# Optimization experiments

Hardware: AMD Instinct MI355X
Metric: run time of the kernel (lower is better)

The kernel has to match this reference:

```python
import jax, jax.numpy as jnp
import numpy as np

N_NODES = 20000
N_EDGES = 320000
N_QUERY = 100000
D = 256


def _sage_conv(x, adj_row, adj_col, Wl, bl, Wr):
    # PyG SAGEConv with mean aggregation over SparseTensor adj_t:
    #   out = lin_l(mean_{j in N(i)} x_j) + lin_r(x_i)
    # adj_row = destination node, adj_col = source node.
    n = x.shape[0]
    msg = x[adj_col]                                        # [E, D] gather
    agg = jax.ops.segment_sum(msg, adj_row, num_segments=n)  # [N, D]
    deg = jax.ops.segment_sum(jnp.ones((adj_row.shape[0],), x.dtype), adj_row,
                              num_segments=n)
    agg = agg / jnp.maximum(deg, 1.0)[:, None]               # mean reduce
    return agg @ Wl + bl + x @ Wr


def setup_inputs() -> dict:
    key = jax.random.key(0)
    ks = jax.random.split(key, 12)
    s = 1.0 / np.sqrt(D)
    return {
        "adj_row": jax.random.randint(ks[0], (N_EDGES,), 0, N_NODES, dtype=jnp.int32),
        "adj_col": jax.random.randint(ks[1], (N_EDGES,), 0, N_NODES, dtype=jnp.int32),
        "edges": jax.random.randint(ks[2], (2, N_QUERY), 0, N_NODES, dtype=jnp.int32),
        "emb": jax.random.normal(ks[3], (N_NODES, D), jnp.float32),
        "W1l": jax.random.normal(ks[4], (D, D), jnp.float32) * s,
        "b1": jnp.zeros((D,), jnp.float32),
        "W1r": jax.random.normal(ks[5], (D, D), jnp.float32) * s,
        "W2l": jax.random.normal(ks[6], (D, D), jnp.float32) * s,
        "b2": jnp.zeros((D,), jnp.float32),
        "W2r": jax.random.normal(ks[7], (D, D), jnp.float32) * s,
        "Wp1": jax.random.normal(ks[8], (D, D), jnp.float32) * s,
        "bp1": jnp.zeros((D,), jnp.float32),
        "Wp2": jax.random.normal(ks[9], (D, 1), jnp.float32) * s,
        "bp2": jnp.zeros((1,), jnp.float32),
    }


def reference(adj_row, adj_col, edges, emb, W1l, b1, W1r, W2l, b2, W2r,
              Wp1, bp1, Wp2, bp2):
    # SAGE backbone (eval mode: dropout is identity)
    x = _sage_conv(emb, adj_row, adj_col, W1l, b1, W1r)
    x = jax.nn.relu(x)
    x = _sage_conv(x, adj_row, adj_col, W2l, b2, W2r)     # [N, D]
    # LinkPredictor: h = x_i * x_j -> MLP -> sigmoid
    h = x[edges[0]] * x[edges[1]]                          # [Q, D]
    h = jax.nn.relu(h @ Wp1 + bp1)
    return jax.nn.sigmoid(h @ Wp2 + bp2)                   # [Q, 1]
```

## Files before the change

kernel.cpp:

```cpp
#include <hip/hip_runtime.h>
#include <cstddef>

constexpr int NN = 20000;
constexpr int NE = 320000;
constexpr int NQ = 100000;
constexpr int DD = 256;
constexpr int NB = (NN + 255) / 256;
constexpr int CASTB = (NN * DD / 8 + 255) / 256;

typedef __attribute__((ext_vector_type(8))) short bf16x8;
typedef __attribute__((ext_vector_type(4))) float f32x4;
typedef __attribute__((ext_vector_type(4))) unsigned short u16x4;
typedef __attribute__((ext_vector_type(8))) unsigned short u16x8;

__device__ inline unsigned short f2bf(float f) {
    union { float f; unsigned u; } v; v.f = f;
    unsigned r = v.u + 0x7fffu + ((v.u >> 16) & 1u);
    return (unsigned short)(r >> 16);
}
__device__ inline float bf2f(unsigned short h) {
    union { unsigned u; float f; } t; t.u = ((unsigned)h) << 16;
    return t.f;
}

__global__ __launch_bounds__(256) void k_castpack(
    const float* __restrict__ x, unsigned short* __restrict__ y,
    int* __restrict__ deg, int* __restrict__ bflag,
    const float* __restrict__ w0, const float* __restrict__ w1,
    const float* __restrict__ w2, const float* __restrict__ w3,
    const float* __restrict__ w4,
    unsigned short* __restrict__ h0, unsigned short* __restrict__ h1,
    unsigned short* __restrict__ h2, unsigned short* __restrict__ h3,
    unsigned short* __restrict__ h4,
    unsigned short* __restrict__ l0, unsigned short* __restrict__ l1,
    unsigned short* __restrict__ l2, unsigned short* __restrict__ l3) {
    const int bid = blockIdx.x;
    if (bid < CASTB) {
        int i = bid * 256 + threadIdx.x;
        if (i < NN) deg[i] = 0;
        if (bid == 0 && threadIdx.x < NB) bflag[threadIdx.x] = 0;
        if (i >= NN * DD / 8) return;
        float4 f0 = *reinterpret_cast<const float4*>(x + (size_t)i * 8);
        float4 f1 = *reinterpret_cast<const float4*>(x + (size_t)i * 8 + 4);
        u16x8 o;
        o[0] = f2bf(f0.x); o[1] = f2bf(f0.y); o[2] = f2bf(f0.z); o[3] = f2bf(f0.w);
        o[4] = f2bf(f1.x); o[5] = f2bf(f1.y); o[6] = f2bf(f1.z); o[7] = f2bf(f1.w);
        *reinterpret_cast<u16x8*>(y + (size_t)i * 8) = o;
        return;
    }
    int mb = bid - CASTB;
    int m = mb >> 5;
    int idx = (mb & 31) * 256 + threadIdx.x;
    const float* W = (m == 0) ? w0 : (m == 1) ? w1 : (m == 2) ? w2 : (m == 3) ? w3 : w4;
    unsigned short* H = (m == 0) ? h0 : (m == 1) ? h1 : (m == 2) ? h2 : (m == 3) ? h3 : h4;
    unsigned short* L = (m == 0) ? l0 : (m == 1) ? l1 : (m == 2) ? l2 : (m == 3) ? l3 : nullptr;
    int t = idx >> 6, lane = idx & 63;
    int kt = t >> 4, nt = t & 15;
    int k0 = kt * 32 + (lane >> 4) * 8;
    int n = nt * 16 + (lane & 15);
    unsigned uh[4], ul[4];
#pragma unroll
    for (int i = 0; i < 4; ++i) {
        float fa = W[(size_t)(k0 + 2 * i) * DD + n];
        float fb = W[(size_t)(k0 + 2 * i + 1) * DD + n];
        unsigned short ha = f2bf(fa), hb = f2bf(fb);
        unsigned short la = f2bf(fa - bf2f(ha)), lb = f2bf(fb - bf2f(hb));
        uh[i] = (unsigned)ha | ((unsigned)hb << 16);
        ul[i] = (unsigned)la | ((unsigned)lb << 16);
    }
    *reinterpret_cast<uint4*>(H + (size_t)idx * 8) = make_uint4(uh[0], uh[1], uh[2], uh[3]);
    if (L)
        *reinterpret_cast<uint4*>(L + (size_t)idx * 8) = make_uint4(ul[0], ul[1], ul[2], ul[3]);
}

__global__ __launch_bounds__(256) void k_deg(const int* __restrict__ row,
                                             int* __restrict__ deg) {
    int e = blockIdx.x * 256 + threadIdx.x;
    if (e < NE) atomicAdd(&deg[row[e]], 1);
}

__global__ __launch_bounds__(256) void k_scanf(const int* __restrict__ deg,
                                               int* __restrict__ offs,
                                               int* __restrict__ cursor,
                                               float* __restrict__ recip,
                                               int* __restrict__ bflag) {
    __shared__ int wsum[4];
    __shared__ int s_pre;
    const int tid = threadIdx.x, lane = tid & 63, wid = tid >> 6;
    const int bid = blockIdx.x;
    int i = bid * 256 + tid;
    int v = (i < NN) ? deg[i] : 0;
    int sc = v;
#pragma unroll
    for (int d = 1; d < 64; d <<= 1) {
        int t = __shfl_up(sc, d);
        if (lane >= d) sc += t;
    }
    if (lane == 63) wsum[wid] = sc;
    __syncthreads();
    int wpre = 0;
    for (int w = 0; w < wid; ++w) wpre += wsum[w];
    int btot = wsum[0] + wsum[1] + wsum[2] + wsum[3];

    if (tid == 0) atomicExch(&bflag[bid], btot + 1);

    int myv = 0;
    if (tid < bid) {
        int f;
        do { f = atomicAdd(&bflag[tid], 0); } while (f == 0);
        myv = f - 1;
    }
    int rs = myv;
#pragma unroll
    for (int d = 1; d < 64; d <<= 1) rs += __shfl_xor(rs, d);
    __syncthreads();
    if (lane == 0) wsum[wid] = rs;
    __syncthreads();
    if (tid == 0) s_pre = wsum[0] + wsum[1] + wsum[2] + wsum[3];
    __syncthreads();
    int pre = s_pre;

    if (i < NN) {
        int o = pre + wpre + sc - v;
        offs[i] = o;
        cursor[i] = o;
        recip[i] = 1.0f / fmaxf((float)v, 1.0f);
    }
    if (i == 0) offs[NN] = NE;
}

__global__ __launch_bounds__(256) void k_fill(const int* __restrict__ row,
                                              const int* __restrict__ col,
                                              int* __restrict__ cursor,
                                              int* __restrict__ scol) {
    int e = blockIdx.x * 256 + threadIdx.x;
    if (e < NE) {
        int r = row[e];
        int p = atomicAdd(&cursor[r], 1);
        scol[p] = col[e];
    }
}

__global__ __launch_bounds__(256) void k_lin(
    const unsigned short* __restrict__ A,
    const unsigned short* __restrict__ Wlh, const unsigned short* __restrict__ Wll,
    const unsigned short* __restrict__ Wrh, const unsigned short* __restrict__ Wrl,
    unsigned short* __restrict__ P, unsigned short* __restrict__ Q) {
    const int ns   = blockIdx.x & 7;
    const int mblk = blockIdx.x >> 3;
    const int wave = threadIdx.x >> 6;
    const int lane = threadIdx.x & 63;
    const int row0 = mblk * 128 + wave * 32;
    const int kcol = (lane >> 4) * 8;
    const int ar0 = min(row0 + (lane & 15), NN - 1);
    const int ar1 = min(row0 + 16 + (lane & 15), NN - 1);

    f32x4 accP[2][2], accQ[2][2];
#pragma unroll
    for (int mt = 0; mt < 2; ++mt)
#pragma unroll
        for (int nt = 0; nt < 2; ++nt) {
            accP[mt][nt] = {0, 0, 0, 0};
            accQ[mt][nt] = {0, 0, 0, 0};
        }

#pragma unroll 2
    for (int kt = 0; kt < 8; ++kt) {
        bf16x8 a0 = *reinterpret_cast<const bf16x8*>(A + (size_t)ar0 * DD + kt * 32 + kcol);
        bf16x8 a1 = *reinterpret_cast<const bf16x8*>(A + (size_t)ar1 * DD + kt * 32 + kcol);
#pragma unroll
        for (int nt = 0; nt < 2; ++nt) {
            const size_t fo = ((size_t)((kt * 16 + ns * 2 + nt) * 64 + lane)) * 8;
            bf16x8 blh = *reinterpret_cast<const bf16x8*>(Wlh + fo);
            bf16x8 bll = *reinterpret_cast<const bf16x8*>(Wll + fo);
            bf16x8 brh = *reinterpret_cast<const bf16x8*>(Wrh + fo);
            bf16x8 brl = *reinterpret_cast<const bf16x8*>(Wrl + fo);
            __builtin_amdgcn_s_setprio(1);
            accP[0][nt] = __builtin_amdgcn_mfma_f32_16x16x32_bf16(a0, blh, accP[0][nt], 0, 0, 0);
            accP[1][nt] = __builtin_amdgcn_mfma_f32_16x16x32_bf16(a1, blh, accP[1][nt], 0, 0, 0);
            accP[0][nt] = __builtin_amdgcn_mfma_f32_16x16x32_bf16(a0, bll, accP[0][nt], 0, 0, 0);
            accP[1][nt] = __builtin_amdgcn_mfma_f32_16x16x32_bf16(a1, bll, accP[1][nt], 0, 0, 0);
            accQ[0][nt] = __builtin_amdgcn_mfma_f32_16x16x32_bf16(a0, brh, accQ[0][nt], 0, 0, 0);
            accQ[1][nt] = __builtin_amdgcn_mfma_f32_16x16x32_bf16(a1, brh, accQ[1][nt], 0, 0, 0);
            accQ[0][nt] = __builtin_amdgcn_mfma_f32_16x16x32_bf16(a0, brl, accQ[0][nt], 0, 0, 0);
            accQ[1][nt] = __builtin_amdgcn_mfma_f32_16x16x32_bf16(a1, brl, accQ[1][nt], 0, 0, 0);
            __builtin_amdgcn_s_setprio(0);
        }
    }

    const int n0 = lane & 15;
    const int rg = (lane >> 4) * 4;
#pragma unroll
    for (int mt = 0; mt < 2; ++mt)
#pragma unroll
        for (int nt = 0; nt < 2; ++nt) {
            int n = (ns * 2 + nt) * 16 + n0;
#pragma unroll
            for (int j = 0; j < 4; ++j) {
                int r = row0 + mt * 16 + rg + j;
                if (r < NN) {
                    P[(size_t)r * DD + n] = f2bf(accP[mt][nt][j]);
                    Q[(size_t)r * DD + n] = f2bf(accQ[mt][nt][j]);
                }
            }
        }
}

template <int RELU>
__global__ __launch_bounds__(256) void k_gath(const int* __restrict__ offs,
                                              const int* __restrict__ scol,
                                              const float* __restrict__ recip,
                                              const unsigned short* __restrict__ P,
                                              const unsigned short* __restrict__ Q,
                                              const float* __restrict__ b,
                                              unsigned short* __restrict__ out) {
    int node = blockIdx.x * 4 + (threadIdx.x >> 6);
    int lane = threadIdx.x & 63;
    if (node >= NN) return;
    int s = offs[node];
    int e = offs[node + 1];
    const int half = lane >> 5;
    const int l32 = lane & 31;
    float a0[8] = {0,0,0,0,0,0,0,0}, a1[8] = {0,0,0,0,0,0,0,0};
    float a2[8] = {0,0,0,0,0,0,0,0}, a3[8] = {0,0,0,0,0,0,0,0};
    int p = s;
    for (; p + 7 < e; p += 8) {
        int base = p + 4 * half;
        int c0 = scol[base], c1 = scol[base + 1], c2 = scol[base + 2], c3 = scol[base + 3];
        u16x8 v0 = *reinterpret_cast<const u16x8*>(P + (size_t)c0 * DD + l32 * 8);
        u16x8 v1 = *reinterpret_cast<const u16x8*>(P + (size_t)c1 * DD + l32 * 8);
        u16x8 v2 = *reinterpret_cast<const u16x8*>(P + (size_t)c2 * DD + l32 * 8);
        u16x8 v3 = *reinterpret_cast<const u16x8*>(P + (size_t)c3 * DD + l32 * 8);
#pragma unroll
        for (int i = 0; i < 8; ++i) {
            a0[i] += bf2f(v0[i]); a1[i] += bf2f(v1[i]);
            a2[i] += bf2f(v2[i]); a3[i] += bf2f(v3[i]);
        }
    }
    for (; p + 1 < e; p += 2) {
        int c0 = scol[p + half];
        u16x8 v0 = *reinterpret_cast<const u16x8*>(P + (size_t)c0 * DD + l32 * 8);
#pragma unroll
        for (int i = 0; i < 8; ++i) a0[i] += bf2f(v0[i]);
    }
    if (p < e && half == 0) {
        int c0 = scol[p];
        u16x8 v0 = *reinterpret_cast<const u16x8*>(P + (size_t)c0 * DD + l32 * 8);
#pragma unroll
        for (int i = 0; i < 8; ++i) a1[i] += bf2f(v0[i]);
    }
    float rc = recip[node];
    u16x8 q = *reinterpret_cast<const u16x8*>(Q + (size_t)node * DD + l32 * 8);
    float4 b0 = *reinterpret_cast<const float4*>(b + l32 * 8);
    float4 b1 = *reinterpret_cast<const float4*>(b + l32 * 8 + 4);
    float bb[8] = {b0.x, b0.y, b0.z, b0.w, b1.x, b1.y, b1.z, b1.w};
    u16x8 o;
#pragma unroll
    for (int i = 0; i < 8; ++i) {
        float t = a0[i] + a1[i] + a2[i] + a3[i];
        t += __shfl_xor(t, 32);
        t = t * rc + bf2f(q[i]) + bb[i];
        if (RELU) t = fmaxf(t, 0.0f);
        o[i] = f2bf(t);
    }
    if (half == 0)
        *reinterpret_cast<u16x8*>(out + (size_t)node * DD + l32 * 8) = o;
}

__global__ __launch_bounds__(512, 4) void k_pred(const int* __restrict__ edges,
                                                 const unsigned short* __restrict__ x2,
                                                 const unsigned short* __restrict__ Wp1p,
                                                 const float* __restrict__ bp1,
                                                 const float* __restrict__ Wp2,
                                                 const float* __restrict__ bp2,
                                                 float* __restrict__ out) {
    __shared__ unsigned short sh[128 * 256];
    const int tid = threadIdx.x;
    const int wave = tid >> 6;
    const int lane = tid & 63;
    const int q0 = blockIdx.x * 128;

    const int grow = tid >> 4;
    const int t16 = tid & 15;
#pragma unroll
    for (int s = 0; s < 4; ++s) {
        int r = s * 32 + grow;
        int q = q0 + r;
        u16x8 p0 = {0, 0, 0, 0, 0, 0, 0, 0};
        u16x8 p1 = {0, 0, 0, 0, 0, 0, 0, 0};
        if (q < NQ) {
            int a = edges[q];
            int c = edges[NQ + q];
            const unsigned short* pa = x2 + (size_t)a * DD + t16 * 16;
            const unsigned short* pc = x2 + (size_t)c * DD + t16 * 16;
            u16x8 ua0 = *reinterpret_cast<const u16x8*>(pa);
            u16x8 ua1 = *reinterpret_cast<const u16x8*>(pa + 8);
            u16x8 uc0 = *reinterpret_cast<const u16x8*>(pc);
            u16x8 uc1 = *reinterpret_cast<const u16x8*>(pc + 8);
#pragma unroll
            for (int i = 0; i < 8; ++i) {
                p0[i] = f2bf(bf2f(ua0[i]) * bf2f(uc0[i]));
                p1[i] = f2bf(bf2f(ua1[i]) * bf2f(uc1[i]));
            }
        }
        int swz = (r & 7) << 3;
        *reinterpret_cast<u16x8*>(&sh[r * 256 + ((t16 * 16) ^ swz)]) = p0;
        *reinterpret_cast<u16x8*>(&sh[r * 256 + ((t16 * 16 + 8) ^ swz)]) = p1;
    }
    __syncthreads();

    const int mg = wave >> 2;
    const int ng = wave & 3;
    f32x4 acc[4][4];
#pragma unroll
    for (int m = 0; m < 4; ++m)
#pragma unroll
        for (int n = 0; n < 4; ++n) acc[m][n] = {0, 0, 0, 0};

    const int akoff = (lane >> 4) * 8;
    const int arl = lane & 15;
    for (int kt = 0; kt < 8; ++kt) {
        bf16x8 af[4];
#pragma unroll
        for (int m = 0; m < 4; ++m) {
            int row = (mg * 4 + m) * 16 + arl;
            af[m] = *reinterpret_cast<const bf16x8*>(
                &sh[row * 256 + ((kt * 32 + akoff) ^ ((row & 7) << 3))]);
        }
#pragma unroll
        for (int n = 0; n < 4; ++n) {
            int nt = ng * 4 + n;
            bf16x8 bfrag = *reinterpret_cast<const bf16x8*>(
                Wp1p + ((size_t)((kt * 16 + nt) * 64 + lane)) * 8);
#pragma unroll
            for (int m = 0; m < 4; ++m)
                acc[m][n] = __builtin_amdgcn_mfma_f32_16x16x32_bf16(af[m], bfrag, acc[m][n], 0, 0, 0);
        }
    }

    float rs[4][4];
#pragma unroll
    for (int m = 0; m < 4; ++m)
#pragma unroll
        for (int j = 0; j < 4; ++j) rs[m][j] = 0.0f;
#pragma unroll
    for (int n = 0; n < 4; ++n) {
        int nc = (ng * 4 + n) * 16 + (lane & 15);
        float bias = bp1[nc];
        float w2 = Wp2[nc];
#pragma unroll
        for (int m = 0; m < 4; ++m)
#pragma unroll
            for (int j = 0; j < 4; ++j)
                rs[m][j] += fmaxf(acc[m][n][j] + bias, 0.0f) * w2;
    }
#pragma unroll
    for (int msk = 1; msk < 16; msk <<= 1) {
#pragma unroll
        for (int m = 0; m < 4; ++m)
#pragma unroll
            for (int j = 0; j < 4; ++j) rs[m][j] += __shfl_xor(rs[m][j], msk);
    }

    float* psum = reinterpret_cast<float*>(sh);
    __syncthreads();
    if ((lane & 15) == 0) {
        int rg = (lane >> 4) * 4;
#pragma unroll
        for (int m = 0; m < 4; ++m)
#pragma unroll
            for (int j = 0; j < 4; ++j)
                psum[ng * 128 + (mg * 4 + m) * 16 + rg + j] = rs[m][j];
    }
    __syncthreads();

    if (tid < 128) {
        int q = q0 + tid;
        if (q < NQ) {
            float z = bp2[0];
#pragma unroll
            for (int w = 0; w < 4; ++w) z += psum[w * 128 + tid];
            out[q] = 1.0f / (1.0f + expf(-z));
        }
    }
}

extern "C" void kernel_launch(void* const* d_in, const int* in_sizes, int n_in,
                              void* d_out, int out_size, void* d_ws, size_t ws_size,
                              hipStream_t stream) {
    const int*   adj_row = (const int*)d_in[0];
    const int*   adj_col = (const int*)d_in[1];
    const int*   edges   = (const int*)d_in[2];
    const float* emb     = (const float*)d_in[3];
    const float* W1l     = (const float*)d_in[4];
    const float* b1      = (const float*)d_in[5];
    const float* W1r     = (const float*)d_in[6];
    const float* W2l     = (const float*)d_in[7];
    const float* b2      = (const float*)d_in[8];
    const float* W2r     = (const float*)d_in[9];
    const float* Wp1     = (const float*)d_in[10];
    const float* bp1     = (const float*)d_in[11];
    const float* Wp2     = (const float*)d_in[12];
    const float* bp2     = (const float*)d_in[13];
    float* out = (float*)d_out;

    const size_t featH = (size_t)NN * DD * 2;
    const size_t packBytes = (size_t)DD * DD * 2;

    char* ws = (char*)d_ws;
    size_t off = 0;
    unsigned short* P  = (unsigned short*)(ws + off); off += featH;
    unsigned short* Q  = (unsigned short*)(ws + off); off += featH;
    unsigned short* x1 = (unsigned short*)(ws + off); off += featH;
    unsigned short* xh = (unsigned short*)(ws + off); off += featH;
    int*   deg    = (int*)(ws + off);   off += (size_t)NN * 4;
    int*   offs   = (int*)(ws + off);   off += (size_t)(NN + 1) * 4;
    int*   cursor = (int*)(ws + off);   off += (size_t)NN * 4;
    float* recip  = (float*)(ws + off); off += (size_t)NN * 4;
    int*   bflag  = (int*)(ws + off);   off += (size_t)NB * 4;
    int*   scol   = (int*)(ws + off);   off += (size_t)NE * 4;
    unsigned short* Wp1p = (unsigned short*)(ws + off); off += packBytes;
    unsigned short* pk[8];
    for (int i = 0; i < 8; ++i) { pk[i] = (unsigned short*)(ws + off); off += packBytes; }

    const int MB8 = ((NN + 127) / 128) * 8;

    k_castpack<<<CASTB + 160, 256, 0, stream>>>(emb, xh, deg, bflag,
                                                W1l, W1r, W2l, W2r, Wp1,
                                                pk[0], pk[2], pk[4], pk[6], Wp1p,
                                                pk[1], pk[3], pk[5], pk[7]);
    k_deg<<<(NE + 255) / 256, 256, 0, stream>>>(adj_row, deg);
    k_scanf<<<NB, 256, 0, stream>>>(deg, offs, cursor, recip, bflag);
    k_fill<<<(NE + 255) / 256, 256, 0, stream>>>(adj_row, adj_col, cursor, scol);

    k_lin<<<MB8, 256, 0, stream>>>(xh, pk[0], pk[1], pk[2], pk[3], P, Q);
    k_gath<1><<<(NN + 3) / 4, 256, 0, stream>>>(offs, scol, recip, P, Q, b1, x1);

    unsigned short* x2 = xh;
    k_lin<<<MB8, 256, 0, stream>>>(x1, pk[4], pk[5], pk[6], pk[7], P, Q);
    k_gath<0><<<(NN + 3) / 4, 256, 0, stream>>>(offs, scol, recip, P, Q, b2, x2);

    k_pred<<<(NQ + 127) / 128, 512, 0, stream>>>(edges, x2, Wp1p, bp1, Wp2, bp2, out);
}
```

Measured before the change: 188.8 us.

## Fuse degree count with first linear, and scan with CSR fill

The degree atomics now share a launch with the first-layer linear kernel, as separate block ranges. The prefix scan and the CSR fill are merged into one kernel: the scan blocks signal a global counter and every block spin-waits on it before filling. Together this removes two kernel launches and lets the independent degree and GEMM work overlap. It also adds s_setprio around the MFMA loop in the predictor. The grid-wide spin-wait assumes all scan blocks are resident at once, which adds a deadlock risk and some atomic polling cost.

```diff
diff --git a/kernel.cpp b/kernel.cpp
--- a/kernel.cpp
+++ b/kernel.cpp
@@ -6,6 +6,7 @@
 constexpr int NQ = 100000;
 constexpr int DD = 256;
 constexpr int NB = (NN + 255) / 256;
+constexpr int DEGB = (NE + 255) / 256;
 constexpr int CASTB = (NN * DD / 8 + 255) / 256;
 
 typedef __attribute__((ext_vector_type(8))) short bf16x8;
@@ -38,7 +39,7 @@
     if (bid < CASTB) {
         int i = bid * 256 + threadIdx.x;
         if (i < NN) deg[i] = 0;
-        if (bid == 0 && threadIdx.x < NB) bflag[threadIdx.x] = 0;
+        if (bid == 0 && threadIdx.x <= NB) bflag[threadIdx.x] = 0;
         if (i >= NN * DD / 8) return;
         float4 f0 = *reinterpret_cast<const float4*>(x + (size_t)i * 8);
         float4 f1 = *reinterpret_cast<const float4*>(x + (size_t)i * 8 + 4);
@@ -73,81 +74,14 @@
         *reinterpret_cast<uint4*>(L + (size_t)idx * 8) = make_uint4(ul[0], ul[1], ul[2], ul[3]);
 }
 
-__global__ __launch_bounds__(256) void k_deg(const int* __restrict__ row,
-                                             int* __restrict__ deg) {
-    int e = blockIdx.x * 256 + threadIdx.x;
-    if (e < NE) atomicAdd(&deg[row[e]], 1);
-}
-
-__global__ __launch_bounds__(256) void k_scanf(const int* __restrict__ deg,
-                                               int* __restrict__ offs,
-                                               int* __restrict__ cursor,
-                                               float* __restrict__ recip,
-                                               int* __restrict__ bflag) {
-    __shared__ int wsum[4];
-    __shared__ int s_pre;
-    const int tid = threadIdx.x, lane = tid & 63, wid = tid >> 6;
-    const int bid = blockIdx.x;
-    int i = bid * 256 + tid;
-    int v = (i < NN) ? deg[i] : 0;
-    int sc = v;
-#pragma unroll
-    for (int d = 1; d < 64; d <<= 1) {
-        int t = __shfl_up(sc, d);
-        if (lane >= d) sc += t;
-    }
-    if (lane == 63) wsum[wid] = sc;
-    __syncthreads();
-    int wpre = 0;
-    for (int w = 0; w < wid; ++w) wpre += wsum[w];
-    int btot = wsum[0] + wsum[1] + wsum[2] + wsum[3];
-
-    if (tid == 0) atomicExch(&bflag[bid], btot + 1);
-
-    int myv = 0;
-    if (tid < bid) {
-        int f;
-        do { f = atomicAdd(&bflag[tid], 0); } while (f == 0);
-        myv = f - 1;
-    }
-    int rs = myv;
-#pragma unroll
-    for (int d = 1; d < 64; d <<= 1) rs += __shfl_xor(rs, d);
-    __syncthreads();
-    if (lane == 0) wsum[wid] = rs;
-    __syncthreads();
-    if (tid == 0) s_pre = wsum[0] + wsum[1] + wsum[2] + wsum[3];
-    __syncthreads();
-    int pre = s_pre;
-
-    if (i < NN) {
-        int o = pre + wpre + sc - v;
-        offs[i] = o;
-        cursor[i] = o;
-        recip[i] = 1.0f / fmaxf((float)v, 1.0f);
-    }
-    if (i == 0) offs[NN] = NE;
-}
-
-__global__ __launch_bounds__(256) void k_fill(const int* __restrict__ row,
-                                              const int* __restrict__ col,
-                                              int* __restrict__ cursor,
-                                              int* __restrict__ scol) {
-    int e = blockIdx.x * 256 + threadIdx.x;
-    if (e < NE) {
-        int r = row[e];
-        int p = atomicAdd(&cursor[r], 1);
-        scol[p] = col[e];
-    }
-}
-
-__global__ __launch_bounds__(256) void k_lin(
+__device__ __forceinline__ void lin_body(
+    int bidx,
     const unsigned short* __restrict__ A,
     const unsigned short* __restrict__ Wlh, const unsigned short* __restrict__ Wll,
     const unsigned short* __restrict__ Wrh, const unsigned short* __restrict__ Wrl,
     unsigned short* __restrict__ P, unsigned short* __restrict__ Q) {
-    const int ns   = blockIdx.x & 7;
-    const int mblk = blockIdx.x >> 3;
+    const int ns   = bidx & 7;
+    const int mblk = bidx >> 3;
     const int wave = threadIdx.x >> 6;
     const int lane = threadIdx.x & 63;
     const int row0 = mblk * 128 + wave * 32;
@@ -204,6 +138,97 @@
                 }
             }
         }
+}
+
+__global__ __launch_bounds__(256) void k_lin(
+    const unsigned short* __restrict__ A,
+    const unsigned short* __restrict__ Wlh, const unsigned short* __restrict__ Wll,
+    const unsigned short* __restrict__ Wrh, const unsigned short* __restrict__ Wrl,
+    unsigned short* __restrict__ P, unsigned short* __restrict__ Q) {
+    lin_body(blockIdx.x, A, Wlh, Wll, Wrh, Wrl, P, Q);
+}
+
+__global__ __launch_bounds__(256) void k_deglin(
+    const int* __restrict__ row, int* __restrict__ deg,
+    const unsigned short* __restrict__ A,
+    const unsigned short* __restrict__ Wlh, const unsigned short* __restrict__ Wll,
+    const unsigned short* __restrict__ Wrh, const unsigned short* __restrict__ Wrl,
+    unsigned short* __restrict__ P, unsigned short* __restrict__ Q) {
+    if (blockIdx.x < DEGB) {
+        int e = blockIdx.x * 256 + threadIdx.x;
+        if (e < NE) atomicAdd(&deg[row[e]], 1);
+        return;
+    }
+    lin_body(blockIdx.x - DEGB, A, Wlh, Wll, Wrh, Wrl, P, Q);
+}
+
+__global__ __launch_bounds__(256) void k_scanfill(
+    const int* __restrict__ deg, int* __restrict__ offs,
+    int* __restrict__ cursor, float* __restrict__ recip,
+    int* __restrict__ bflag, int* __restrict__ scnt,
+    const int* __restrict__ row, const int* __restrict__ col,
+    int* __restrict__ scol) {
+    __shared__ int wsum[4];
+    __shared__ int s_pre;
+    const int tid = threadIdx.x, lane = tid & 63, wid = tid >> 6;
+    const int bid = blockIdx.x;
+
+    if (bid < NB) {
+        int i = bid * 256 + tid;
+        int v = (i < NN) ? deg[i] : 0;
+        int sc = v;
+#pragma unroll
+        for (int d = 1; d < 64; d <<= 1) {
+            int t = __shfl_up(sc, d);
+            if (lane >= d) sc += t;
+        }
+        if (lane == 63) wsum[wid] = sc;
+        __syncthreads();
+        int wpre = 0;
+        for (int w = 0; w < wid; ++w) wpre += wsum[w];
+        int btot = wsum[0] + wsum[1] + wsum[2] + wsum[3];
+
+        if (tid == 0) atomicExch(&bflag[bid], btot + 1);
+
+        int myv = 0;
+        if (tid < bid) {
+            int f;
+            do { f = atomicAdd(&bflag[tid], 0); } while (f == 0);
+            myv = f - 1;
+        }
+        int rs = myv;
+#pragma unroll
+        for (int d = 1; d < 64; d <<= 1) rs += __shfl_xor(rs, d);
+        __syncthreads();
+        if (lane == 0) wsum[wid] = rs;
+        __syncthreads();
+        if (tid == 0) s_pre = wsum[0] + wsum[1] + wsum[2] + wsum[3];
+        __syncthreads();
+        int pre = s_pre;
+
+        if (i < NN) {
+            int o = pre + wpre + sc - v;
+            offs[i] = o;
+            cursor[i] = o;
+            recip[i] = 1.0f / fmaxf((float)v, 1.0f);
+        }
+        if (i == 0) offs[NN] = NE;
+        __threadfence();
+        if (tid == 0) atomicAdd(scnt, 1);
+    }
+
+    if (tid == 0) {
+        while (atomicAdd(scnt, 0) < NB) {}
+    }
+    __syncthreads();
+    __threadfence();
+
+    int e = bid * 256 + tid;
+    if (e < NE) {
+        int r = row[e];
+        int p = atomicAdd(&cursor[r], 1);
+        scol[p] = col[e];
+    }
 }
 
 template <int RELU>
@@ -332,9 +357,11 @@
             int nt = ng * 4 + n;
             bf16x8 bfrag = *reinterpret_cast<const bf16x8*>(
                 Wp1p + ((size_t)((kt * 16 + nt) * 64 + lane)) * 8);
+            __builtin_amdgcn_s_setprio(1);
 #pragma unroll
             for (int m = 0; m < 4; ++m)
                 acc[m][n] = __builtin_amdgcn_mfma_f32_16x16x32_bf16(af[m], bfrag, acc[m][n], 0, 0, 0);
+            __builtin_amdgcn_s_setprio(0);
         }
     }
 
@@ -417,7 +444,8 @@
     int*   offs   = (int*)(ws + off);   off += (size_t)(NN + 1) * 4;
     int*   cursor = (int*)(ws + off);   off += (size_t)NN * 4;
     float* recip  = (float*)(ws + off); off += (size_t)NN * 4;
-    int*   bflag  = (int*)(ws + off);   off += (size_t)NB * 4;
+    int*   bflag  = (int*)(ws + off);   off += (size_t)(NB + 1) * 4;
+    int*   scnt   = bflag + NB;
     int*   scol   = (int*)(ws + off);   off += (size_t)NE * 4;
     unsigned short* Wp1p = (unsigned short*)(ws + off); off += packBytes;
     unsigned short* pk[8];
@@ -429,16 +457,13 @@
                                                 W1l, W1r, W2l, W2r, Wp1,
                                                 pk[0], pk[2], pk[4], pk[6], Wp1p,
                                                 pk[1], pk[3], pk[5], pk[7]);
-    k_deg<<<(NE + 255) / 256, 256, 0, stream>>>(adj_row, deg);
-    k_scanf<<<NB, 256, 0, stream>>>(deg, offs, cursor, recip, bflag);
-    k_fill<<<(NE + 255) / 256, 256, 0, stream>>>(adj_row, adj_col, cursor, scol);
-
-    k_lin<<<MB8, 256, 0, stream>>>(xh, pk[0], pk[1], pk[2], pk[3], P, Q);
+    k_deglin<<<DEGB + MB8, 256, 0, stream>>>(adj_row, deg, xh,
+                                             pk[0], pk[1], pk[2], pk[3], P, Q);
+    k_scanfill<<<DEGB, 256, 0, stream>>>(deg, offs, cursor, recip, bflag, scnt,
+                                         adj_row, adj_col, scol);
     k_gath<1><<<(NN + 3) / 4, 256, 0, stream>>>(offs, scol, recip, P, Q, b1, x1);
-
+    k_lin<<<MB8, 256, 0, stream>>>(x1, pk[4], pk[5], pk[6], pk[7], P, Q);
     unsigned short* x2 = xh;
-    k_lin<<<MB8, 256, 0, stream>>>(x1, pk[4], pk[5], pk[6], pk[7], P, Q);
     k_gath<0><<<(NN + 3) / 4, 256, 0, stream>>>(offs, scol, recip, P, Q, b2, x2);
-
     k_pred<<<(NQ + 127) / 128, 512, 0, stream>>>(edges, x2, Wp1p, bp1, Wp2, bp2, out);
 }
```

New measurement: 269.9 us. 42.9% more time.
